# Kernel tuning notes

Hardware: AMD Instinct MI355X
Metric: run time of the kernel (lower is better)

## Reference

```python
import jax, jax.numpy as jnp
import numpy as np

N_NODES = 100000
N_EDGES = 1600000
FDIM = 128


def setup_inputs() -> dict:
    key = jax.random.key(0)
    k1, k2 = jax.random.split(key)
    x = jax.random.normal(k1, (N_NODES, FDIM), dtype=jnp.float32)
    edge_index = jax.random.randint(k2, (2, N_EDGES), 0, N_NODES, dtype=jnp.int64)
    # GCNConv params as loaded by the module: identity weight, zero bias
    W = jnp.eye(FDIM, dtype=jnp.float32)
    bias = jnp.zeros((FDIM,), dtype=jnp.float32)
    return {"x": x, "W": W, "bias": bias, "edge_index": edge_index}


def reference(x, W, bias, edge_index):
    n = x.shape[0]
    src, dst = edge_index[0], edge_index[1]
    # GCNConv default: add self-loops with weight 1.0
    loop = jnp.arange(n, dtype=edge_index.dtype)
    src_f = jnp.concatenate([src, loop])
    dst_f = jnp.concatenate([dst, loop])
    ew = jnp.ones(src_f.shape[0], dtype=x.dtype)
    # symmetric normalization: deg computed on destination (col)
    deg = jax.ops.segment_sum(ew, dst_f, num_segments=n)
    dinv = jnp.where(deg > 0, deg ** -0.5, 0.0).astype(x.dtype)
    norm = dinv[src_f] * dinv[dst_f]  # [E+n]
    h = x @ W.T  # linear transform (W = I here, but kept faithful)
    msg = h[src_f] * norm[:, None]  # gather + scale, [E+n, fdim]
    out = jax.ops.segment_sum(msg, dst_f, num_segments=n) + bias  # scatter-add
    return jnp.sum(out, axis=0, keepdims=True)  # [1, fdim]
```

## Files before the change

### kernel.cpp

```cpp
#include <hip/hip_runtime.h>

#define FD 128
#define CHD 32768
#define NSLD 64
#define CHS 16384
#define NSLS 64
#define RXB 512
#define QSCALE 16777216.0f
#define QINV   5.9604644775390625e-8f

__device__ __forceinline__ unsigned quant_w(int dp1) {
    return (unsigned)(rsqrtf((float)dp1) * QSCALE + 0.5f);
}

__device__ __forceinline__ bool detect_is32(const unsigned int* w, unsigned int* sflag,
                                            int tid, int nthr, int kmax) {
    if (tid == 0) *sflag = 0u;
    __syncthreads();
    unsigned acc = 0;
    for (int k = tid; k < kmax; k += nthr) acc |= w[2 * k + 1];
    if (acc) atomicOr(sflag, 1u);
    __syncthreads();
    return *sflag != 0u;
}

__global__ void convert_kernel(const unsigned int* __restrict__ w64,
                               int* __restrict__ e32, long long total) {
    __shared__ unsigned int sflag;
    int kmax = (int)((total / 2 < 256) ? total / 2 : 256);
    bool is32 = detect_is32(w64, &sflag, threadIdx.x, blockDim.x, kmax);
    if (is32) return;
    const long long* e64 = (const long long*)w64;
    const long long R = ((total + gridDim.x - 1) / gridDim.x + 1) & ~1LL;
    const long long base = (long long)blockIdx.x * R;
    long long end = base + R; if (end > total) end = total;
    for (long long i = base + (long long)threadIdx.x * 2; i + 1 < end;
         i += (long long)blockDim.x * 2) {
        longlong2 v = *reinterpret_cast<const longlong2*>(e64 + i);
        *reinterpret_cast<int2*>(e32 + i) = make_int2((int)v.x, (int)v.y);
    }
}

__global__ __launch_bounds__(512) void hist_deg_kernel(
        const void* __restrict__ ei, const int* __restrict__ e32,
        unsigned int* __restrict__ psD, long long E, long long SL, int nch) {
    __shared__ unsigned int hist[CHD / 2];
    __shared__ unsigned int sflag;
    const int tid = threadIdx.x;
    const bool is32 = detect_is32((const unsigned int*)ei, &sflag, tid, 512, 256);
    const int* DST = (is32 ? (const int*)ei : e32) + E;
    const int b = blockIdx.x;
    const int c = b % nch;
    const int j = b / nch;
    const int lo = c * CHD;
    for (int i = tid; i < CHD / 2; i += 512) hist[i] = 0u;
    __syncthreads();
    const long long e0 = (long long)j * SL;
    long long e1 = e0 + SL; if (e1 > E) e1 = E; if (e1 < e0) e1 = e0;
    const long long e1v = e0 + ((e1 - e0) & ~3LL);
    for (long long i = e0 + (long long)tid * 4; i < e1v; i += 2048) {
        int4 d = *reinterpret_cast<const int4*>(DST + i);
        unsigned u0 = (unsigned)(d.x - lo), u1 = (unsigned)(d.y - lo);
        unsigned u2 = (unsigned)(d.z - lo), u3 = (unsigned)(d.w - lo);
        if (u0 < CHD) atomicAdd(&hist[u0 >> 1], 1u << ((u0 & 1) * 16));
        if (u1 < CHD) atomicAdd(&hist[u1 >> 1], 1u << ((u1 & 1) * 16));
        if (u2 < CHD) atomicAdd(&hist[u2 >> 1], 1u << ((u2 & 1) * 16));
        if (u3 < CHD) atomicAdd(&hist[u3 >> 1], 1u << ((u3 & 1) * 16));
    }
    { long long it = e1v + tid;
      if (it < e1) { unsigned u = (unsigned)(DST[it] - lo);
                     if (u < CHD) atomicAdd(&hist[u >> 1], 1u << ((u & 1) * 16)); } }
    __syncthreads();
    unsigned int* o = psD + (size_t)b * (CHD / 2);
    for (int w = tid; w < CHD / 2; w += 512) o[w] = hist[w];
}

__global__ void deg_reduce_kernel(const unsigned int* __restrict__ psD,
                                  int* __restrict__ deg, long long n, int nch) {
    const long long tw = blockIdx.x * (long long)blockDim.x + threadIdx.x;
    const long long nwords = (long long)nch * (CHD / 2);
    if (tw >= nwords) return;
    const int cc = (int)(tw / (CHD / 2));
    const int w  = (int)(tw % (CHD / 2));
    unsigned s0 = 0, s1 = 0;
    for (int j = 0; j < NSLD; ++j) {
        unsigned v = psD[((size_t)j * nch + cc) * (CHD / 2) + w];
        s0 += v & 0xffffu; s1 += v >> 16;
    }
    const long long v0 = (long long)cc * CHD + 2 * w;
    if (v0 < n) deg[v0] = (int)s0;
    if (v0 + 1 < n) deg[v0 + 1] = (int)s1;
}

__global__ __launch_bounds__(512) void hist_s_kernel(
        const void* __restrict__ ei, const int* __restrict__ e32,
        const int* __restrict__ deg, unsigned int* __restrict__ psS,
        long long E, long long SL, int nch) {
    __shared__ unsigned int hist[CHS];
    __shared__ unsigned int sflag;
    const int tid = threadIdx.x;
    const bool is32 = detect_is32((const unsigned int*)ei, &sflag, tid, 512, 256);
    const int* SRC = is32 ? (const int*)ei : e32;
    const int* DST = SRC + E;
    const int b = blockIdx.x;
    const int c = b % nch;
    const int j = b / nch;
    const int lo = c * CHS;
    for (int i = tid; i < CHS; i += 512) hist[i] = 0u;
    __syncthreads();
    const long long e0 = (long long)j * SL;
    long long e1 = e0 + SL; if (e1 > E) e1 = E; if (e1 < e0) e1 = e0;
    const long long e1v = e0 + ((e1 - e0) & ~3LL);
    for (long long i = e0 + (long long)tid * 4; i < e1v; i += 2048) {
        int4 s = *reinterpret_cast<const int4*>(SRC + i);
        int4 d = *reinterpret_cast<const int4*>(DST + i);
        unsigned u0 = (unsigned)(s.x - lo), u1 = (unsigned)(s.y - lo);
        unsigned u2 = (unsigned)(s.z - lo), u3 = (unsigned)(s.w - lo);
        if (u0 < CHS) atomicAdd(&hist[u0], quant_w(deg[d.x] + 1));
        if (u1 < CHS) atomicAdd(&hist[u1], quant_w(deg[d.y] + 1));
        if (u2 < CHS) atomicAdd(&hist[u2], quant_w(deg[d.z] + 1));
        if (u3 < CHS) atomicAdd(&hist[u3], quant_w(deg[d.w] + 1));
    }
    { long long it = e1v + tid;
      if (it < e1) { unsigned u = (unsigned)(SRC[it] - lo);
                     if (u < CHS) atomicAdd(&hist[u], quant_w(deg[DST[it]] + 1)); } }
    __syncthreads();
    unsigned int* o = psS + (size_t)b * CHS;
    for (int w = tid; w < CHS; w += 512) o[w] = hist[w];
}

__global__ void coef_reduce_kernel(const unsigned int* __restrict__ psS,
                                   const int* __restrict__ deg,
                                   float* __restrict__ coef, long long n, int nch) {
    const long long v = blockIdx.x * (long long)blockDim.x + threadIdx.x;
    if (v >= n) return;
    const int cc = (int)(v / CHS);
    const int u  = (int)(v % CHS);
    unsigned s = 0;
    for (int jj = 0; jj < NSLS; ++jj)
        s += psS[((size_t)jj * nch + cc) * CHS + u];
    const float dg = (float)(deg[v] + 1);
    const float di = rsqrtf(dg);
    coef[v] = di * ((float)s * QINV) + 1.0f / dg;
}

__global__ __launch_bounds__(256) void reduce_x_kernel(
        const float* __restrict__ x, const float* __restrict__ coef,
        float* __restrict__ P, long long n) {
    __shared__ float4 sm4[256];
    const int tid = threadIdx.x;
    float4 a = make_float4(0.f, 0.f, 0.f, 0.f);
    const long long tot = n * (FD / 4);
    for (long long i = blockIdx.x * 256LL + tid; i < tot; i += (long long)RXB * 256) {
        float cf = coef[i >> 5];
        float4 xv = reinterpret_cast<const float4*>(x)[i];
        a.x += cf * xv.x; a.y += cf * xv.y; a.z += cf * xv.z; a.w += cf * xv.w;
    }
    const int lane = tid & 31, grp = tid >> 5;
    sm4[grp * 32 + lane] = a;
    __syncthreads();
    for (int s2 = 4; s2 > 0; s2 >>= 1) {
        if (grp < s2) {
            float4 o = sm4[(grp + s2) * 32 + lane];
            float4 m = sm4[grp * 32 + lane];
            m.x += o.x; m.y += o.y; m.z += o.z; m.w += o.w;
            sm4[grp * 32 + lane] = m;
        }
        __syncthreads();
    }
    if (tid < 32) reinterpret_cast<float4*>(P)[blockIdx.x * 32 + tid] = sm4[tid];
}

__global__ __launch_bounds__(256) void colsum_final_kernel(
        const float* __restrict__ P, const float* __restrict__ Wm,
        const float* __restrict__ bias, float* __restrict__ out, float nn) {
    __shared__ float wrow[FD];
    __shared__ float red[256];
    const int f = blockIdx.x, tid = threadIdx.x;
    if (tid < FD) wrow[tid] = Wm[f * FD + tid];
    __syncthreads();
    float part = 0.f;
    for (int j = tid; j < RXB; j += 256) {
        const float4* Pj = reinterpret_cast<const float4*>(P + (size_t)j * FD);
        #pragma unroll
        for (int k = 0; k < FD / 4; ++k) {
            float4 p = Pj[k];
            part += wrow[4 * k] * p.x + wrow[4 * k + 1] * p.y +
                    wrow[4 * k + 2] * p.z + wrow[4 * k + 3] * p.w;
        }
    }
    red[tid] = part;
    __syncthreads();
    for (int s2 = 128; s2 > 0; s2 >>= 1) {
        if (tid < s2) red[tid] += red[tid + s2];
        __syncthreads();
    }
    if (tid == 0) out[f] = red[0] + nn * bias[f];
}

__global__ void deg_fb(const void* __restrict__ ei, int* __restrict__ deg, long long E) {
    __shared__ unsigned int sflag;
    int kmax = (int)((E < 256) ? (E > 1 ? E - 1 : 1) : 256);
    bool is32 = detect_is32((const unsigned int*)ei, &sflag, threadIdx.x, blockDim.x, kmax);
    const long long st = (long long)gridDim.x * blockDim.x;
    long long i = blockIdx.x * (long long)blockDim.x + threadIdx.x;
    if (is32) { const int* D = (const int*)ei + E;
        for (; i < E; i += st) atomicAdd(&deg[D[i]], 1);
    } else { const long long* D = (const long long*)ei + E;
        for (; i < E; i += st) atomicAdd(&deg[(int)D[i]], 1);
    }
}

__global__ void srcsum_fb(const void* __restrict__ ei, const int* __restrict__ deg,
                          unsigned int* __restrict__ Sq, long long E) {
    __shared__ unsigned int sflag;
    int kmax = (int)((E < 256) ? (E > 1 ? E - 1 : 1) : 256);
    bool is32 = detect_is32((const unsigned int*)ei, &sflag, threadIdx.x, blockDim.x, kmax);
    const long long st = (long long)gridDim.x * blockDim.x;
    long long i = blockIdx.x * (long long)blockDim.x + threadIdx.x;
    if (is32) { const int* S = (const int*)ei; const int* D = S + E;
        for (; i < E; i += st) atomicAdd(&Sq[S[i]], quant_w(deg[D[i]] + 1));
    } else { const long long* S = (const long long*)ei; const long long* D = S + E;
        for (; i < E; i += st) atomicAdd(&Sq[(int)S[i]], quant_w(deg[(int)D[i]] + 1));
    }
}

__global__ void coef_fb(unsigned int* __restrict__ Sq, const int* __restrict__ deg,
                        long long n) {
    const long long v = blockIdx.x * (long long)blockDim.x + threadIdx.x;
    if (v >= n) return;
    unsigned s = Sq[v];
    float dg = (float)(deg[v] + 1);
    float di = rsqrtf(dg);
    ((float*)Sq)[v] = di * ((float)s * QINV) + 1.0f / dg;
}

__global__ void redx_fb(const float* __restrict__ x, const float* __restrict__ coef,
                        float* __restrict__ t, long long n) {
    __shared__ float sm[FD];
    for (int f = threadIdx.x; f < FD; f += blockDim.x) sm[f] = 0.f;
    __syncthreads();
    const long long tot = n * (FD / 4);
    const long long st = (long long)gridDim.x * blockDim.x;
    const int lane = threadIdx.x & 31;
    float4 a = make_float4(0.f, 0.f, 0.f, 0.f);
    for (long long i = blockIdx.x * (long long)blockDim.x + threadIdx.x; i < tot; i += st) {
        float cf = coef[i >> 5];
        float4 xv = reinterpret_cast<const float4*>(x)[i];
        a.x += cf * xv.x; a.y += cf * xv.y; a.z += cf * xv.z; a.w += cf * xv.w;
    }
    atomicAdd(&sm[lane * 4 + 0], a.x);
    atomicAdd(&sm[lane * 4 + 1], a.y);
    atomicAdd(&sm[lane * 4 + 2], a.z);
    atomicAdd(&sm[lane * 4 + 3], a.w);
    __syncthreads();
    for (int f = threadIdx.x; f < FD; f += blockDim.x) atomicAdd(&t[f], sm[f]);
}

__global__ void final_fb(const float* __restrict__ Wm, const float* __restrict__ bias,
                         const float* __restrict__ t, float* __restrict__ out, float nn) {
    __shared__ float ts[FD];
    int f = threadIdx.x;
    if (f < FD) ts[f] = t[f];
    __syncthreads();
    if (f < FD) {
        float a0 = 0.f;
        #pragma unroll 16
        for (int k = 0; k < FD; ++k) a0 += Wm[f * FD + k] * ts[k];
        out[f] = a0 + nn * bias[f];
    }
}

extern "C" void kernel_launch(void* const* d_in, const int* in_sizes, int n_in,
                              void* d_out, int out_size, void* d_ws, size_t ws_size,
                              hipStream_t stream) {
    const float* x    = (const float*)d_in[0];
    const float* W    = (const float*)d_in[1];
    const float* bias = (const float*)d_in[2];
    const void*  ei   = d_in[3];
    float* out = (float*)d_out;
    const long long n = in_sizes[0] / FD;
    const long long E = (long long)in_sizes[3] / 2;

    const int NCHD = (int)((n + CHD - 1) / CHD);
    const int NCHS = (int)((n + CHS - 1) / CHS);
    const long long SLD = ((E + NSLD - 1) / NSLD + 3) & ~3LL;
    const long long SLS = ((E + NSLS - 1) / NSLS + 3) & ~3LL;
    const bool u16_ok = (SLD < 65536);

    char* ws = (char*)d_ws;
    size_t off = 0;
    auto take = [&](size_t bytes) { size_t r = off; off += (bytes + 255) & ~(size_t)255; return r; };
    int*          e32  = (int*)(ws + take((size_t)2 * E * 4));
    unsigned int* psD  = (unsigned int*)(ws + take((size_t)NCHD * NSLD * (CHD / 2) * 4));
    unsigned int* psS  = (unsigned int*)(ws + take((size_t)NCHS * NSLS * CHS * 4));
    int*          deg  = (int*)(ws + take((size_t)n * 4));
    float*        coef = (float*)(ws + take((size_t)n * 4));
    float*        P    = (float*)(ws + take((size_t)RXB * FD * 4));
    const size_t need = off;

    const bool main_ok = (ws_size >= need) && ((E & 3) == 0) && (E >= 512) && u16_ok;

    if (main_ok) {
        convert_kernel<<<512, 256, 0, stream>>>((const unsigned int*)ei, e32, 2 * E);
        hist_deg_kernel<<<NCHD * NSLD, 512, 0, stream>>>(ei, e32, psD, E, SLD, NCHD);
        {
            long long nw = (long long)NCHD * (CHD / 2);
            deg_reduce_kernel<<<(int)((nw + 255) / 256), 256, 0, stream>>>(psD, deg, n, NCHD);
        }
        hist_s_kernel<<<NCHS * NSLS, 512, 0, stream>>>(ei, e32, deg, psS, E, SLS, NCHS);
        coef_reduce_kernel<<<(int)((n + 255) / 256), 256, 0, stream>>>(psS, deg, coef, n, NCHS);
        reduce_x_kernel<<<RXB, 256, 0, stream>>>(x, coef, P, n);
        colsum_final_kernel<<<FD, 256, 0, stream>>>(P, W, bias, out, (float)n);
    } else {
        int*          degF = (int*)ws;
        unsigned int* Sq   = (unsigned int*)(ws + (size_t)n * 4);
        float*        tF   = (float*)(ws + (size_t)n * 8);
        hipMemsetAsync(ws, 0, (size_t)n * 8 + 512, stream);
        deg_fb<<<1600, 256, 0, stream>>>(ei, degF, E);
        srcsum_fb<<<1600, 256, 0, stream>>>(ei, degF, Sq, E);
        coef_fb<<<(int)((n + 255) / 256), 256, 0, stream>>>(Sq, degF, n);
        redx_fb<<<2048, 256, 0, stream>>>(x, (const float*)Sq, tF, n);
        final_fb<<<1, FD, 0, stream>>>(W, bias, tF, out, (float)n);
    }
}
```

Before: 86.71 us.

## Drop int64 conversion pass, fuse coef reduce and final colsum into reduce kernel

Removes the separate int64-to-int32 edge conversion kernel by having the histogram kernels read int64 indices directly, and detects the index width per wave with a ballot instead of a block barrier. Fuses the per-node coefficient reduction into the x-reduction kernel, with each lane reading one slice partial and combining them by shuffle; NSLS is set to 32 to match the lane count. A last-block-done atomic counter folds the final column sum and W multiply into the same kernel. This cuts three launches and a full pass over the edge array, at the cost of wider int64 loads in both histogram passes and redundant psS reads spread across lanes.

```diff
diff --git a/kernel.cpp b/kernel.cpp
--- a/kernel.cpp
+++ b/kernel.cpp
@@ -4,8 +4,9 @@
 #define CHD 32768
 #define NSLD 64
 #define CHS 16384
-#define NSLS 64
-#define RXB 512
+#define NSLS 32
+#define RXB 256
+#define RXT 512
 #define QSCALE 16777216.0f
 #define QINV   5.9604644775390625e-8f
 
@@ -13,45 +14,34 @@
     return (unsigned)(rsqrtf((float)dp1) * QSCALE + 0.5f);
 }
 
-__device__ __forceinline__ bool detect_is32(const unsigned int* w, unsigned int* sflag,
-                                            int tid, int nthr, int kmax) {
-    if (tid == 0) *sflag = 0u;
-    __syncthreads();
+__device__ __forceinline__ bool detect_is32_wave(const unsigned int* w, long long nwords) {
+    const int lane = threadIdx.x & 63;
+    const long long i0 = 2 * lane + 1, i1 = 2 * (lane + 64) + 1;
     unsigned acc = 0;
-    for (int k = tid; k < kmax; k += nthr) acc |= w[2 * k + 1];
-    if (acc) atomicOr(sflag, 1u);
-    __syncthreads();
-    return *sflag != 0u;
-}
-
-__global__ void convert_kernel(const unsigned int* __restrict__ w64,
-                               int* __restrict__ e32, long long total) {
-    __shared__ unsigned int sflag;
-    int kmax = (int)((total / 2 < 256) ? total / 2 : 256);
-    bool is32 = detect_is32(w64, &sflag, threadIdx.x, blockDim.x, kmax);
-    if (is32) return;
-    const long long* e64 = (const long long*)w64;
-    const long long R = ((total + gridDim.x - 1) / gridDim.x + 1) & ~1LL;
-    const long long base = (long long)blockIdx.x * R;
-    long long end = base + R; if (end > total) end = total;
-    for (long long i = base + (long long)threadIdx.x * 2; i + 1 < end;
-         i += (long long)blockDim.x * 2) {
-        longlong2 v = *reinterpret_cast<const longlong2*>(e64 + i);
-        *reinterpret_cast<int2*>(e32 + i) = make_int2((int)v.x, (int)v.y);
-    }
+    if (i0 < nwords) acc |= w[i0];
+    if (i1 < nwords) acc |= w[i1];
+    return __ballot(acc != 0u) != 0ull;
+}
+
+__device__ __forceinline__ int4 ld_e4(const void* ei, bool is32, long long off, long long i) {
+    if (is32) return *reinterpret_cast<const int4*>((const int*)ei + off + i);
+    const long long* p = (const long long*)ei + off + i;
+    longlong2 a = *reinterpret_cast<const longlong2*>(p);
+    longlong2 b = *reinterpret_cast<const longlong2*>(p + 2);
+    return make_int4((int)a.x, (int)a.y, (int)b.x, (int)b.y);
+}
+__device__ __forceinline__ int ld_e1(const void* ei, bool is32, long long idx) {
+    return is32 ? ((const int*)ei)[idx] : (int)((const long long*)ei)[idx];
 }
 
 __global__ __launch_bounds__(512) void hist_deg_kernel(
-        const void* __restrict__ ei, const int* __restrict__ e32,
-        unsigned int* __restrict__ psD, long long E, long long SL, int nch) {
+        const void* __restrict__ ei, unsigned int* __restrict__ psD,
+        unsigned int* __restrict__ counter, long long E, long long SL, int nch) {
     __shared__ unsigned int hist[CHD / 2];
-    __shared__ unsigned int sflag;
     const int tid = threadIdx.x;
-    const bool is32 = detect_is32((const unsigned int*)ei, &sflag, tid, 512, 256);
-    const int* DST = (is32 ? (const int*)ei : e32) + E;
-    const int b = blockIdx.x;
-    const int c = b % nch;
-    const int j = b / nch;
+    if (blockIdx.x == 0 && tid == 0) *counter = 0u;
+    const bool is32 = detect_is32_wave((const unsigned int*)ei, 2 * E);
+    const int b = blockIdx.x, c = b % nch, j = b / nch;
     const int lo = c * CHD;
     for (int i = tid; i < CHD / 2; i += 512) hist[i] = 0u;
     __syncthreads();
@@ -59,7 +49,7 @@
     long long e1 = e0 + SL; if (e1 > E) e1 = E; if (e1 < e0) e1 = e0;
     const long long e1v = e0 + ((e1 - e0) & ~3LL);
     for (long long i = e0 + (long long)tid * 4; i < e1v; i += 2048) {
-        int4 d = *reinterpret_cast<const int4*>(DST + i);
+        int4 d = ld_e4(ei, is32, E, i);
         unsigned u0 = (unsigned)(d.x - lo), u1 = (unsigned)(d.y - lo);
         unsigned u2 = (unsigned)(d.z - lo), u3 = (unsigned)(d.w - lo);
         if (u0 < CHD) atomicAdd(&hist[u0 >> 1], 1u << ((u0 & 1) * 16));
@@ -68,7 +58,7 @@
         if (u3 < CHD) atomicAdd(&hist[u3 >> 1], 1u << ((u3 & 1) * 16));
     }
     { long long it = e1v + tid;
-      if (it < e1) { unsigned u = (unsigned)(DST[it] - lo);
+      if (it < e1) { unsigned u = (unsigned)(ld_e1(ei, is32, E + it) - lo);
                      if (u < CHD) atomicAdd(&hist[u >> 1], 1u << ((u & 1) * 16)); } }
     __syncthreads();
     unsigned int* o = psD + (size_t)b * (CHD / 2);
@@ -78,8 +68,7 @@
 __global__ void deg_reduce_kernel(const unsigned int* __restrict__ psD,
                                   int* __restrict__ deg, long long n, int nch) {
     const long long tw = blockIdx.x * (long long)blockDim.x + threadIdx.x;
-    const long long nwords = (long long)nch * (CHD / 2);
-    if (tw >= nwords) return;
+    if (tw >= (long long)nch * (CHD / 2)) return;
     const int cc = (int)(tw / (CHD / 2));
     const int w  = (int)(tw % (CHD / 2));
     unsigned s0 = 0, s1 = 0;
@@ -93,18 +82,12 @@
 }
 
 __global__ __launch_bounds__(512) void hist_s_kernel(
-        const void* __restrict__ ei, const int* __restrict__ e32,
-        const int* __restrict__ deg, unsigned int* __restrict__ psS,
-        long long E, long long SL, int nch) {
+        const void* __restrict__ ei, const int* __restrict__ deg,
+        unsigned int* __restrict__ psS, long long E, long long SL, int nch) {
     __shared__ unsigned int hist[CHS];
-    __shared__ unsigned int sflag;
     const int tid = threadIdx.x;
-    const bool is32 = detect_is32((const unsigned int*)ei, &sflag, tid, 512, 256);
-    const int* SRC = is32 ? (const int*)ei : e32;
-    const int* DST = SRC + E;
-    const int b = blockIdx.x;
-    const int c = b % nch;
-    const int j = b / nch;
+    const bool is32 = detect_is32_wave((const unsigned int*)ei, 2 * E);
+    const int b = blockIdx.x, c = b % nch, j = b / nch;
     const int lo = c * CHS;
     for (int i = tid; i < CHS; i += 512) hist[i] = 0u;
     __syncthreads();
@@ -112,8 +95,8 @@
     long long e1 = e0 + SL; if (e1 > E) e1 = E; if (e1 < e0) e1 = e0;
     const long long e1v = e0 + ((e1 - e0) & ~3LL);
     for (long long i = e0 + (long long)tid * 4; i < e1v; i += 2048) {
-        int4 s = *reinterpret_cast<const int4*>(SRC + i);
-        int4 d = *reinterpret_cast<const int4*>(DST + i);
+        int4 s = ld_e4(ei, is32, 0, i);
+        int4 d = ld_e4(ei, is32, E, i);
         unsigned u0 = (unsigned)(s.x - lo), u1 = (unsigned)(s.y - lo);
         unsigned u2 = (unsigned)(s.z - lo), u3 = (unsigned)(s.w - lo);
         if (u0 < CHS) atomicAdd(&hist[u0], quant_w(deg[d.x] + 1));
@@ -122,107 +105,96 @@
         if (u3 < CHS) atomicAdd(&hist[u3], quant_w(deg[d.w] + 1));
     }
     { long long it = e1v + tid;
-      if (it < e1) { unsigned u = (unsigned)(SRC[it] - lo);
-                     if (u < CHS) atomicAdd(&hist[u], quant_w(deg[DST[it]] + 1)); } }
+      if (it < e1) { unsigned u = (unsigned)(ld_e1(ei, is32, it) - lo);
+                     if (u < CHS) atomicAdd(&hist[u], quant_w(deg[ld_e1(ei, is32, E + it)] + 1)); } }
     __syncthreads();
     unsigned int* o = psS + (size_t)b * CHS;
     for (int w = tid; w < CHS; w += 512) o[w] = hist[w];
 }
 
-__global__ void coef_reduce_kernel(const unsigned int* __restrict__ psS,
-                                   const int* __restrict__ deg,
-                                   float* __restrict__ coef, long long n, int nch) {
-    const long long v = blockIdx.x * (long long)blockDim.x + threadIdx.x;
-    if (v >= n) return;
-    const int cc = (int)(v / CHS);
-    const int u  = (int)(v % CHS);
-    unsigned s = 0;
-    for (int jj = 0; jj < NSLS; ++jj)
-        s += psS[((size_t)jj * nch + cc) * CHS + u];
-    const float dg = (float)(deg[v] + 1);
-    const float di = rsqrtf(dg);
-    coef[v] = di * ((float)s * QINV) + 1.0f / dg;
-}
-
-__global__ __launch_bounds__(256) void reduce_x_kernel(
-        const float* __restrict__ x, const float* __restrict__ coef,
-        float* __restrict__ P, long long n) {
-    __shared__ float4 sm4[256];
+__global__ __launch_bounds__(RXT) void reduce_x_final_kernel(
+        const float* __restrict__ x, const int* __restrict__ deg,
+        const unsigned int* __restrict__ psS, const float* __restrict__ Wm,
+        const float* __restrict__ bias, float* __restrict__ P,
+        unsigned int* __restrict__ counter, float* __restrict__ out,
+        long long n, int nchs) {
+    __shared__ float4 sm4[RXT];
     const int tid = threadIdx.x;
+    const int lane = tid & 31;
+    const int grp = tid >> 5;
     float4 a = make_float4(0.f, 0.f, 0.f, 0.f);
     const long long tot = n * (FD / 4);
-    for (long long i = blockIdx.x * 256LL + tid; i < tot; i += (long long)RXB * 256) {
-        float cf = coef[i >> 5];
-        float4 xv = reinterpret_cast<const float4*>(x)[i];
-        a.x += cf * xv.x; a.y += cf * xv.y; a.z += cf * xv.z; a.w += cf * xv.w;
-    }
-    const int lane = tid & 31, grp = tid >> 5;
-    sm4[grp * 32 + lane] = a;
-    __syncthreads();
-    for (int s2 = 4; s2 > 0; s2 >>= 1) {
+    for (long long i = blockIdx.x * (long long)RXT + tid; i < tot;
+         i += (long long)RXB * RXT) {
+        const long long v = i >> 5;
+        const int cc = (int)(v / CHS);
+        const int u  = (int)(v % CHS);
+        unsigned s = psS[((size_t)lane * nchs + cc) * CHS + u];
+        #pragma unroll
+        for (int m = 1; m < 32; m <<= 1)
+            s += (unsigned)__shfl_xor((int)s, m, 32);
+        const float dg = (float)(deg[v] + 1);
+        const float di = rsqrtf(dg);
+        const float coef = di * ((float)s * QINV) + 1.0f / dg;
+        const float4 xv = reinterpret_cast<const float4*>(x)[i];
+        a.x += coef * xv.x; a.y += coef * xv.y; a.z += coef * xv.z; a.w += coef * xv.w;
+    }
+    sm4[tid] = a;
+    __syncthreads();
+    for (int s2 = 8; s2 > 0; s2 >>= 1) {
         if (grp < s2) {
             float4 o = sm4[(grp + s2) * 32 + lane];
-            float4 m = sm4[grp * 32 + lane];
+            float4 m = sm4[tid];
             m.x += o.x; m.y += o.y; m.z += o.z; m.w += o.w;
-            sm4[grp * 32 + lane] = m;
+            sm4[tid] = m;
         }
         __syncthreads();
     }
     if (tid < 32) reinterpret_cast<float4*>(P)[blockIdx.x * 32 + tid] = sm4[tid];
-}
-
-__global__ __launch_bounds__(256) void colsum_final_kernel(
-        const float* __restrict__ P, const float* __restrict__ Wm,
-        const float* __restrict__ bias, float* __restrict__ out, float nn) {
-    __shared__ float wrow[FD];
-    __shared__ float red[256];
-    const int f = blockIdx.x, tid = threadIdx.x;
-    if (tid < FD) wrow[tid] = Wm[f * FD + tid];
-    __syncthreads();
-    float part = 0.f;
-    for (int j = tid; j < RXB; j += 256) {
-        const float4* Pj = reinterpret_cast<const float4*>(P + (size_t)j * FD);
-        #pragma unroll
-        for (int k = 0; k < FD / 4; ++k) {
-            float4 p = Pj[k];
-            part += wrow[4 * k] * p.x + wrow[4 * k + 1] * p.y +
-                    wrow[4 * k + 2] * p.z + wrow[4 * k + 3] * p.w;
-        }
-    }
-    red[tid] = part;
-    __syncthreads();
-    for (int s2 = 128; s2 > 0; s2 >>= 1) {
-        if (tid < s2) red[tid] += red[tid + s2];
-        __syncthreads();
-    }
-    if (tid == 0) out[f] = red[0] + nn * bias[f];
+    __threadfence();
+    __shared__ unsigned last;
+    if (tid == 0) {
+        unsigned old = atomicAdd(counter, 1u);
+        last = (old == RXB - 1) ? 1u : 0u;
+        if (last) atomicExch(counter, 0u);
+    }
+    __syncthreads();
+    if (last == 0u) return;
+    __threadfence();
+    __shared__ float tcol[FD];
+    __shared__ float part[RXT];
+    const int k = tid & (FD - 1);
+    const int q = tid >> 7;
+    float ps = 0.f;
+    for (int j = q * (RXB / 4); j < (q + 1) * (RXB / 4); ++j)
+        ps += __hip_atomic_load(&P[(size_t)j * FD + k], __ATOMIC_RELAXED,
+                                __HIP_MEMORY_SCOPE_AGENT);
+    part[tid] = ps;
+    __syncthreads();
+    if (tid < FD) tcol[tid] = part[tid] + part[tid + 128] + part[tid + 256] + part[tid + 384];
+    __syncthreads();
+    if (tid < FD) {
+        float acc = 0.f;
+        #pragma unroll 16
+        for (int kk = 0; kk < FD; ++kk) acc += Wm[tid * FD + kk] * tcol[kk];
+        out[tid] = acc + (float)n * bias[tid];
+    }
 }
 
 __global__ void deg_fb(const void* __restrict__ ei, int* __restrict__ deg, long long E) {
-    __shared__ unsigned int sflag;
-    int kmax = (int)((E < 256) ? (E > 1 ? E - 1 : 1) : 256);
-    bool is32 = detect_is32((const unsigned int*)ei, &sflag, threadIdx.x, blockDim.x, kmax);
+    const bool is32 = detect_is32_wave((const unsigned int*)ei, 2 * E);
     const long long st = (long long)gridDim.x * blockDim.x;
     long long i = blockIdx.x * (long long)blockDim.x + threadIdx.x;
-    if (is32) { const int* D = (const int*)ei + E;
-        for (; i < E; i += st) atomicAdd(&deg[D[i]], 1);
-    } else { const long long* D = (const long long*)ei + E;
-        for (; i < E; i += st) atomicAdd(&deg[(int)D[i]], 1);
-    }
+    for (; i < E; i += st) atomicAdd(&deg[ld_e1(ei, is32, E + i)], 1);
 }
 
 __global__ void srcsum_fb(const void* __restrict__ ei, const int* __restrict__ deg,
                           unsigned int* __restrict__ Sq, long long E) {
-    __shared__ unsigned int sflag;
-    int kmax = (int)((E < 256) ? (E > 1 ? E - 1 : 1) : 256);
-    bool is32 = detect_is32((const unsigned int*)ei, &sflag, threadIdx.x, blockDim.x, kmax);
+    const bool is32 = detect_is32_wave((const unsigned int*)ei, 2 * E);
     const long long st = (long long)gridDim.x * blockDim.x;
     long long i = blockIdx.x * (long long)blockDim.x + threadIdx.x;
-    if (is32) { const int* S = (const int*)ei; const int* D = S + E;
-        for (; i < E; i += st) atomicAdd(&Sq[S[i]], quant_w(deg[D[i]] + 1));
-    } else { const long long* S = (const long long*)ei; const long long* D = S + E;
-        for (; i < E; i += st) atomicAdd(&Sq[(int)S[i]], quant_w(deg[(int)D[i]] + 1));
-    }
+    for (; i < E; i += st)
+        atomicAdd(&Sq[ld_e1(ei, is32, i)], quant_w(deg[ld_e1(ei, is32, E + i)] + 1));
 }
 
 __global__ void coef_fb(unsigned int* __restrict__ Sq, const int* __restrict__ deg,
@@ -286,32 +258,29 @@
     const int NCHS = (int)((n + CHS - 1) / CHS);
     const long long SLD = ((E + NSLD - 1) / NSLD + 3) & ~3LL;
     const long long SLS = ((E + NSLS - 1) / NSLS + 3) & ~3LL;
-    const bool u16_ok = (SLD < 65536);
 
     char* ws = (char*)d_ws;
     size_t off = 0;
     auto take = [&](size_t bytes) { size_t r = off; off += (bytes + 255) & ~(size_t)255; return r; };
-    int*          e32  = (int*)(ws + take((size_t)2 * E * 4));
-    unsigned int* psD  = (unsigned int*)(ws + take((size_t)NCHD * NSLD * (CHD / 2) * 4));
-    unsigned int* psS  = (unsigned int*)(ws + take((size_t)NCHS * NSLS * CHS * 4));
-    int*          deg  = (int*)(ws + take((size_t)n * 4));
-    float*        coef = (float*)(ws + take((size_t)n * 4));
-    float*        P    = (float*)(ws + take((size_t)RXB * FD * 4));
+    unsigned int* psD     = (unsigned int*)(ws + take((size_t)NCHD * NSLD * (CHD / 2) * 4));
+    unsigned int* psS     = (unsigned int*)(ws + take((size_t)NCHS * NSLS * CHS * 4));
+    int*          deg     = (int*)(ws + take((size_t)n * 4));
+    float*        P       = (float*)(ws + take((size_t)RXB * FD * 4));
+    unsigned int* counter = (unsigned int*)(ws + take(256));
     const size_t need = off;
 
-    const bool main_ok = (ws_size >= need) && ((E & 3) == 0) && (E >= 512) && u16_ok;
+    const bool main_ok = (ws_size >= need) && ((E & 3) == 0) && (E >= 512) &&
+                         (SLD < 65536);
 
     if (main_ok) {
-        convert_kernel<<<512, 256, 0, stream>>>((const unsigned int*)ei, e32, 2 * E);
-        hist_deg_kernel<<<NCHD * NSLD, 512, 0, stream>>>(ei, e32, psD, E, SLD, NCHD);
+        hist_deg_kernel<<<NCHD * NSLD, 512, 0, stream>>>(ei, psD, counter, E, SLD, NCHD);
         {
             long long nw = (long long)NCHD * (CHD / 2);
             deg_reduce_kernel<<<(int)((nw + 255) / 256), 256, 0, stream>>>(psD, deg, n, NCHD);
         }
-        hist_s_kernel<<<NCHS * NSLS, 512, 0, stream>>>(ei, e32, deg, psS, E, SLS, NCHS);
-        coef_reduce_kernel<<<(int)((n + 255) / 256), 256, 0, stream>>>(psS, deg, coef, n, NCHS);
-        reduce_x_kernel<<<RXB, 256, 0, stream>>>(x, coef, P, n);
-        colsum_final_kernel<<<FD, 256, 0, stream>>>(P, W, bias, out, (float)n);
+        hist_s_kernel<<<NCHS * NSLS, 512, 0, stream>>>(ei, deg, psS, E, SLS, NCHS);
+        reduce_x_final_kernel<<<RXB, RXT, 0, stream>>>(x, deg, psS, W, bias, P,
+                                                       counter, out, n, NCHS);
     } else {
         int*          degF = (int*)ws;
         unsigned int* Sq   = (unsigned int*)(ws + (size_t)n * 4);
```

Result: slower. 130.7 us (+50.7%).
